# Optimization experiments

Hardware: AMD Instinct MI355X
Metric: run time of the kernel (lower is better)

## Reference

```python
import jax, jax.numpy as jnp
import numpy as np
from jax import lax

H_SIZE = 2048
NUM_K = 16
NUM_V = 32
DK = 128
DV = 128
KDIM = NUM_K * DK      # 2048
VDIM = NUM_V * DV      # 4096
KCONV = 4
RMS_EPS = 1e-6
L2_EPS = 1e-6


def l2norm(x, eps=L2_EPS):
    # matches torch l2norm: x * rsqrt(sum(x^2, -1) + eps)
    return x * lax.rsqrt(jnp.sum(x * x, axis=-1, keepdims=True) + eps)


def setup_inputs() -> dict:
    key = jax.random.key(0)
    ks = jax.random.split(key, 7)
    B, S = 2, 1024
    conv_dim = 2 * KDIM + VDIM  # 8192
    return {
        "hidden_states": jax.random.normal(ks[0], (B, S, H_SIZE), jnp.float32),
        "w_qkvz": jax.random.normal(ks[1], (H_SIZE, 2 * KDIM + 2 * VDIM), jnp.float32) * 0.02,
        "w_ba": jax.random.normal(ks[2], (H_SIZE, 2 * NUM_V), jnp.float32) * 0.02,
        "conv_w": jax.random.normal(ks[3], (conv_dim, 1, KCONV), jnp.float32) * 0.2,  # depthwise [C,1,K]
        "dt_bias": jnp.ones((NUM_V,), jnp.float32),
        "A_log": jnp.log(jax.random.uniform(ks[4], (NUM_V,), jnp.float32, 0.5, 8.0)),
        "norm_w": jnp.ones((DV,), jnp.float32),
        "w_out": jax.random.normal(ks[5], (VDIM, H_SIZE), jnp.float32) * 0.02,
    }


def _forward(hidden_states, w_qkvz, w_ba, conv_w, dt_bias, A_log, norm_w, w_out):
    B, S, _ = hidden_states.shape
    rf = NUM_V // NUM_K  # GQA repeat factor = 2

    # input projections
    qkvz = hidden_states @ w_qkvz                                  # [B,S,12288]
    ba = hidden_states @ w_ba                                      # [B,S,64]

    # fix_query_key_value_ordering: group per k-head then split
    qkvz = qkvz.reshape(B, S, NUM_K, 2 * DK + 2 * rf * DV)
    q, k, v, z = jnp.split(qkvz, [DK, 2 * DK, 2 * DK + rf * DV], axis=3)
    ba = ba.reshape(B, S, NUM_K, 2 * rf)
    b, a = jnp.split(ba, [rf], axis=3)
    v = v.reshape(B, S, NUM_V, DV)
    z = z.reshape(B, S, NUM_V, DV)
    b = b.reshape(B, S, NUM_V)
    a = a.reshape(B, S, NUM_V)

    # depthwise causal conv over [q|k|v] channels + silu
    mixed = jnp.concatenate(
        [q.reshape(B, S, KDIM), k.reshape(B, S, KDIM), v.reshape(B, S, VDIM)], axis=-1
    )                                                              # [B,S,conv_dim]
    x = mixed.transpose(0, 2, 1)                                   # [B,C,S]
    x = jnp.pad(x, ((0, 0), (0, 0), (KCONV - 1, 0)))
    x = lax.conv_general_dilated(x, conv_w, window_strides=(1,), padding="VALID",
                                 feature_group_count=x.shape[1])
    x = jax.nn.silu(x).transpose(0, 2, 1)                          # [B,S,conv_dim]

    q, k, v = jnp.split(x, [KDIM, 2 * KDIM], axis=-1)
    q = q.reshape(B, S, NUM_K, DK)
    k = k.reshape(B, S, NUM_K, DK)
    v = v.reshape(B, S, NUM_V, DV)

    beta = jax.nn.sigmoid(b)                                       # [B,S,NUM_V]
    g = -jnp.exp(A_log) * jax.nn.softplus(a + dt_bias)             # log-decay [B,S,NUM_V]

    if rf > 1:
        q = jnp.repeat(q, rf, axis=2)                              # [B,S,NUM_V,DK]
        k = jnp.repeat(k, rf, axis=2)
    q = l2norm(q) * (DK ** -0.5)
    k = l2norm(k)

    # gated delta rule recurrence over time via lax.scan
    S0 = jnp.zeros((B, NUM_V, DK, DV), q.dtype)

    def step(state, inp):
        q_t, k_t, v_t, g_t, b_t = inp                              # [B,H,dk]/[B,H,dv]/[B,H]
        state = state * jnp.exp(g_t)[..., None, None]              # decay
        kv_mem = jnp.einsum("bhkv,bhk->bhv", state, k_t)
        delta = (v_t - kv_mem) * b_t[..., None]
        state = state + jnp.einsum("bhk,bhv->bhkv", k_t, delta)
        o = jnp.einsum("bhkv,bhk->bhv", state, q_t)
        return state, o

    xs = (jnp.moveaxis(q, 1, 0), jnp.moveaxis(k, 1, 0), jnp.moveaxis(v, 1, 0),
          jnp.moveaxis(g, 1, 0), jnp.moveaxis(beta, 1, 0))
    _, out = lax.scan(step, S0, xs)
    out = jnp.moveaxis(out, 0, 1)                                  # [B,S,NUM_V,DV]

    # gated RMSNorm (gate applied before normalization, Mamba2 style)
    xg = out * jax.nn.silu(z)
    y = xg * lax.rsqrt(jnp.mean(xg * xg, axis=-1, keepdims=True) + RMS_EPS) * norm_w
    y = y.reshape(B, S, VDIM)
    return y @ w_out                                               # [B,S,H_SIZE]


def reference(hidden_states, w_qkvz, w_ba, conv_w, dt_bias, A_log, norm_w, w_out):
    return _forward(hidden_states, w_qkvz, w_ba, conv_w, dt_bias, A_log, norm_w, w_out)
```

## Files before the change

### kernel.cpp

```cpp
#include <hip/hip_runtime.h>
#include <stdint.h>

#define AS1 __attribute__((address_space(1)))
#define AS3 __attribute__((address_space(3)))

typedef __bf16 bf16x8 __attribute__((ext_vector_type(8)));
typedef float f32x4 __attribute__((ext_vector_type(4)));

static __device__ __forceinline__ float bf2f(unsigned short u) {
    union { unsigned int i; float f; } x; x.i = ((unsigned int)u) << 16; return x.f;
}
static __device__ __forceinline__ unsigned short f2bf(float f) {
    union { float f; unsigned int i; } x; x.f = f;
    unsigned int u = x.i;
    unsigned int r = (u + 0x7fffu + ((u >> 16) & 1u)) >> 16;
    return (unsigned short)r;
}

static __device__ __forceinline__ void gll16(const void* g, void* l) {
    __builtin_amdgcn_global_load_lds((const AS1 unsigned int*)g,
                                     (AS3 unsigned int*)l, 16, 0, 0);
}

__global__ __launch_bounds__(256) void cvt_bf16_kernel(
    const float* __restrict__ src, unsigned short* __restrict__ dst, int n4) {
    int i = blockIdx.x * 256 + threadIdx.x;
    if (i >= n4) return;
    float4 v = ((const float4*)src)[i];
    ushort4 o;
    o.x = f2bf(v.x); o.y = f2bf(v.y); o.z = f2bf(v.z); o.w = f2bf(v.w);
    ((ushort4*)dst)[i] = o;
}

__global__ __launch_bounds__(256) void transpose_cvt_kernel(
    const float* __restrict__ src, unsigned short* __restrict__ dst, int R, int C) {
    __shared__ float tile[32][33];
    int x = threadIdx.x & 31, y = threadIdx.x >> 5;
    int c0 = blockIdx.x * 32, r0 = blockIdx.y * 32;
#pragma unroll
    for (int i = 0; i < 4; i++)
        tile[y + i * 8][x] = src[(size_t)(r0 + y + i * 8) * C + (c0 + x)];
    __syncthreads();
#pragma unroll
    for (int i = 0; i < 4; i++)
        dst[(size_t)(c0 + y + i * 8) * R + (r0 + x)] = f2bf(tile[x][y + i * 8]);
}

template <int STORE_BF16>
__global__ __launch_bounds__(256) void gemm_bt_kernel(
    const unsigned short* __restrict__ A, const unsigned short* __restrict__ Bt,
    void* __restrict__ C, int M, int N, int K) {
    __shared__ __align__(16) unsigned short As[128 * 32];
    __shared__ __align__(16) unsigned short Bs[128 * 32];
    int tid = threadIdx.x;
    int lane = tid & 63;
    int w = tid >> 6;
    int m0 = blockIdx.y * 128;
    int n0 = blockIdx.x * 128;
    int qd = lane >> 4, rc = lane & 15;
    int wm = (w >> 1) * 64, wn = (w & 1) * 64;

    f32x4 acc[4][4];
#pragma unroll
    for (int i = 0; i < 4; i++)
#pragma unroll
        for (int j = 0; j < 4; j++)
#pragma unroll
            for (int r = 0; r < 4; r++) acc[i][j][r] = 0.f;

    int s0 = w * 128 + lane;
    int s1 = s0 + 64;
    int rA0 = s0 >> 2, cs0 = (s0 & 3) * 8;
    int rA1 = s1 >> 2, cs1 = (s1 & 3) * 8;
    const unsigned short* a0 = A + (size_t)(m0 + rA0) * K + cs0;
    const unsigned short* a1 = A + (size_t)(m0 + rA1) * K + cs1;
    const unsigned short* b0 = Bt + (size_t)(n0 + rA0) * K + cs0;
    const unsigned short* b1 = Bt + (size_t)(n0 + rA1) * K + cs1;
    unsigned short* lA0 = As + s0 * 8;
    unsigned short* lA1 = As + s1 * 8;
    unsigned short* lB0 = Bs + s0 * 8;
    unsigned short* lB1 = Bs + s1 * 8;

    for (int k0 = 0; k0 < K; k0 += 32) {
        __syncthreads();
        gll16(a0 + k0, lA0);
        gll16(a1 + k0, lA1);
        gll16(b0 + k0, lB0);
        gll16(b1 + k0, lB1);
        __syncthreads();
        bf16x8 af[4], bfr[4];
#pragma unroll
        for (int i = 0; i < 4; i++)
            af[i] = *(const bf16x8*)(As + (wm + i * 16 + rc) * 32 + qd * 8);
#pragma unroll
        for (int i = 0; i < 4; i++)
            bfr[i] = *(const bf16x8*)(Bs + (wn + i * 16 + rc) * 32 + qd * 8);
#pragma unroll
        for (int i = 0; i < 4; i++)
#pragma unroll
            for (int j = 0; j < 4; j++)
                acc[i][j] = __builtin_amdgcn_mfma_f32_16x16x32_bf16(af[i], bfr[j], acc[i][j], 0, 0, 0);
    }

#pragma unroll
    for (int i = 0; i < 4; i++)
#pragma unroll
        for (int j = 0; j < 4; j++)
#pragma unroll
            for (int r = 0; r < 4; r++) {
                int row = m0 + wm + i * 16 + qd * 4 + r;
                int col = n0 + wn + j * 16 + rc;
                if (STORE_BF16)
                    ((unsigned short*)C)[(size_t)row * N + col] = f2bf(acc[i][j][r]);
                else
                    ((float*)C)[(size_t)row * N + col] = acc[i][j][r];
            }
}

__global__ __launch_bounds__(256) void bag_kernel(
    const float* __restrict__ hs, const float* __restrict__ w_ba,
    const float* __restrict__ A_log, const float* __restrict__ dt_bias,
    float* __restrict__ gg, float* __restrict__ bb) {
    int w = threadIdx.x >> 6, lane = threadIdx.x & 63;
    int r0 = blockIdx.x * 8 + w * 2;
    const float* h0 = hs + (size_t)r0 * 2048;
    float a0 = 0.f, a1 = 0.f;
    for (int k = 0; k < 2048; k++) {
        float wv = w_ba[k * 64 + lane];
        a0 += h0[k] * wv;
        a1 += h0[2048 + k] * wv;
    }
    int h = lane >> 2, idx = lane & 3;
    int vh = h * 2 + (idx & 1);
    float accs[2] = {a0, a1};
#pragma unroll
    for (int j = 0; j < 2; j++) {
        int t = r0 + j;
        float acc = accs[j];
        if (idx < 2) {
            bb[t * 32 + vh] = 1.f / (1.f + expf(-acc));
        } else {
            float x = acc + dt_bias[vh];
            float sp = fmaxf(x, 0.f) + log1pf(expf(-fabsf(x)));
            gg[t * 32 + vh] = -expf(A_log[vh]) * sp;
        }
    }
}

__global__ __launch_bounds__(256) void conv_kernel(
    const unsigned short* __restrict__ qkvz, const float* __restrict__ conv_w,
    unsigned short* __restrict__ qb, unsigned short* __restrict__ kb,
    float* __restrict__ vv) {
    __shared__ float xs[8192];
    __shared__ float rs[32];
    int t = blockIdx.x;
    int s = t & 1023;
    int tid = threadIdx.x;
    size_t rowbase = (size_t)t * 12288;
#pragma unroll
    for (int i = 0; i < 4; i++) {
        int c = (i * 256 + tid) * 8;
        int d = c & 127;
        int col;
        if (c < 2048) col = (c >> 7) * 768 + d;
        else if (c < 4096) col = ((c - 2048) >> 7) * 768 + 128 + d;
        else { int vh2 = (c - 4096) >> 7; col = (vh2 >> 1) * 768 + 256 + (vh2 & 1) * 128 + d; }
        float wts[8][4];
#pragma unroll
        for (int e = 0; e < 8; e++) {
            float4 t4 = *(const float4*)(conv_w + (size_t)(c + e) * 4);
            wts[e][0] = t4.x; wts[e][1] = t4.y; wts[e][2] = t4.z; wts[e][3] = t4.w;
        }
        float acc[8] = {0.f, 0.f, 0.f, 0.f, 0.f, 0.f, 0.f, 0.f};
#pragma unroll
        for (int j = 0; j < 4; j++) {
            int ss = s - 3 + j;
            if (ss >= 0) {
                uint4 u = *(const uint4*)(qkvz + rowbase + (size_t)(j - 3) * 12288 + col);
                const unsigned short* us = (const unsigned short*)&u;
#pragma unroll
                for (int e = 0; e < 8; e++) acc[e] += bf2f(us[e]) * wts[e][j];
            }
        }
#pragma unroll
        for (int e = 0; e < 8; e++) xs[c + e] = acc[e] / (1.f + expf(-acc[e]));
    }
    __syncthreads();
    {
        int seg = tid >> 3, part = tid & 7;
        const float* pp = xs + seg * 128 + part * 16;
        float s2 = 0.f;
#pragma unroll
        for (int j = 0; j < 16; j++) s2 += pp[j] * pp[j];
        s2 += __shfl_xor(s2, 1);
        s2 += __shfl_xor(s2, 2);
        s2 += __shfl_xor(s2, 4);
        if (part == 0) rs[seg] = rsqrtf(s2 + 1e-6f);
    }
    __syncthreads();
    const float QS = 0.08838834764831845f;
#pragma unroll
    for (int i = 0; i < 4; i++) {
        int c = (i * 256 + tid) * 8;
        float x[8];
#pragma unroll
        for (int e = 0; e < 8; e++) x[e] = xs[c + e];
        if (c < 4096) {
            float sc = (c < 2048) ? rs[c >> 7] * QS : rs[((c - 2048) >> 7) + 16];
            uint4 o;
            o.x = (unsigned)f2bf(x[0] * sc) | ((unsigned)f2bf(x[1] * sc) << 16);
            o.y = (unsigned)f2bf(x[2] * sc) | ((unsigned)f2bf(x[3] * sc) << 16);
            o.z = (unsigned)f2bf(x[4] * sc) | ((unsigned)f2bf(x[5] * sc) << 16);
            o.w = (unsigned)f2bf(x[6] * sc) | ((unsigned)f2bf(x[7] * sc) << 16);
            if (c < 2048) *(uint4*)(qb + (size_t)t * 2048 + c) = o;
            else *(uint4*)(kb + (size_t)t * 2048 + c - 2048) = o;
        } else {
            float* vp = vv + (size_t)t * 4096 + c - 4096;
            *(float4*)vp = make_float4(x[0], x[1], x[2], x[3]);
            *(float4*)(vp + 4) = make_float4(x[4], x[5], x[6], x[7]);
        }
    }
}

__global__ __launch_bounds__(256, 2) void prep_kernel(
    const unsigned short* __restrict__ qb, const unsigned short* __restrict__ kb,
    const float* __restrict__ vv, const float* __restrict__ gg,
    const float* __restrict__ bb,
    unsigned short* __restrict__ Wg, unsigned short* __restrict__ DlT,
    unsigned short* __restrict__ KtT, unsigned short* __restrict__ Pt,
    float* __restrict__ lamg, float* __restrict__ l64g) {
    __shared__ __align__(16) unsigned short Ks[64 * 136];
    __shared__ __align__(16) unsigned short Tb[64 * 72];
    __shared__ __align__(16) unsigned short Xb[64 * 72];
    __shared__ float Td[4 * 16 * 17];
    __shared__ float RHS[64 * 68];
    __shared__ float cc[64], bet[64], lam_s[64], ex64[64];

    int bid = blockIdx.x;
    int ch = bid & 15, bh = bid >> 4;
    int vh = bh & 31, b = bh >> 5;
    int hk = vh >> 1;
    int t0 = b * 1024 + ch * 64;
    int tid = threadIdx.x, wv = tid >> 6, lane = tid & 63;
    int qd = lane >> 4, rc = lane & 15;
    int rowb = (wv & 1) * 32;
    size_t obase = (size_t)bid * 8192;
    size_t pbase = (size_t)bid * 4096;

    {
        int tok = tid >> 2, seg = (tid & 3) * 32;
        const unsigned short* src = kb + ((size_t)(t0 + tok) * 16 + hk) * 128 + seg;
#pragma unroll
        for (int j = 0; j < 4; j++) {
            uint4 u = *(const uint4*)(src + j * 8);
            *(uint4*)&Ks[tok * 136 + seg + j * 8] = u;
        }
    }
    if (tid < 64) {
        float x = gg[(size_t)(t0 + tid) * 32 + vh];
#pragma unroll
        for (int ofs = 1; ofs < 64; ofs <<= 1) {
            float up = __shfl_up(x, ofs, 64);
            if (tid >= ofs) x += up;
        }
        cc[tid] = x;
        float l = __expf(x);
        lam_s[tid] = l;
        float tot = __shfl(x, 63, 64);
        ex64[tid] = __expf(tot - x);
        bet[tid] = bb[(size_t)(t0 + tid) * 32 + vh];
        lamg[(size_t)bid * 64 + tid] = l;
        if (tid == 0) l64g[bid] = __expf(tot);
    }
    __syncthreads();

    {
        f32x4 acc[2][4];
#pragma unroll
        for (int tm = 0; tm < 2; tm++)
#pragma unroll
            for (int tn = 0; tn < 4; tn++)
#pragma unroll
                for (int r = 0; r < 4; r++) acc[tm][tn][r] = 0.f;
#pragma unroll
        for (int ks = 0; ks < 4; ks++) {
            bf16x8 af[2], bfr[4];
#pragma unroll
            for (int tm = 0; tm < 2; tm++) {
                int row = rowb + tm * 16 + rc;
                if (wv < 2)
                    af[tm] = *(const bf16x8*)&Ks[row * 136 + ks * 32 + qd * 8];
                else
                    af[tm] = *(const bf16x8*)(qb + ((size_t)(t0 + row) * 16 + hk) * 128 + ks * 32 + qd * 8);
            }
#pragma unroll
            for (int tn = 0; tn < 4; tn++)
                bfr[tn] = *(const bf16x8*)&Ks[(tn * 16 + rc) * 136 + ks * 32 + qd * 8];
#pragma unroll
            for (int tm = 0; tm < 2; tm++)
#pragma unroll
                for (int tn = 0; tn < 4; tn++)
                    acc[tm][tn] = __builtin_amdgcn_mfma_f32_16x16x32_bf16(af[tm], bfr[tn], acc[tm][tn], 0, 0, 0);
        }
        if (wv < 2) {
#pragma unroll
            for (int tm = 0; tm < 2; tm++)
#pragma unroll
                for (int tn = 0; tn < 4; tn++)
#pragma unroll
                    for (int r = 0; r < 4; r++) {
                        int i = rowb + tm * 16 + qd * 4 + r;
                        int j = tn * 16 + rc;
                        float val = acc[tm][tn][r];
                        float tv = 0.f;
                        if (i > j) tv = bet[i] * __expf(cc[i] - cc[j]) * val;
                        Tb[i * 72 + j] = f2bf(-tv);
                        if ((i >> 4) == (j >> 4) && i > j)
                            Td[(i >> 4) * 272 + (i & 15) * 17 + (j & 15)] = tv;
                    }
        } else {
#pragma unroll
            for (int tm = 0; tm < 2; tm++)
#pragma unroll
                for (int tn = 0; tn < 4; tn++)
#pragma unroll
                    for (int r = 0; r < 4; r++) {
                        int i = rowb + tm * 16 + qd * 4 + r;
                        int j = tn * 16 + rc;
                        float ev = (i >= j) ? __expf(cc[i] - cc[j]) : 0.f;
                        Pt[pbase + i * 64 + j] = f2bf(ev * acc[tm][tn][r]);
                    }
        }
    }
    {
        int dk = tid >> 1, half = tid & 1;
#pragma unroll
        for (int j = 0; j < 4; j++) {
            unsigned short tmp[8];
#pragma unroll
            for (int e = 0; e < 8; e++) {
                int tok = half * 32 + j * 8 + e;
                tmp[e] = f2bf(bf2f(Ks[tok * 136 + dk]) * ex64[tok]);
            }
            *(uint4*)(KtT + obase + dk * 64 + half * 32 + j * 8) = *(const uint4*)tmp;
        }
    }
    __syncthreads();

#pragma unroll 1
    for (int cb = 0; cb < 4; cb++) {
        for (int z = tid; z < 64 * 72 / 2; z += 256) ((unsigned int*)Xb)[z] = 0u;
        {
            int tok = tid >> 2, c0 = (tid & 3) * 16;
            if (cb < 2) {
                const float* vp = vv + ((size_t)(t0 + tok) * 32 + vh) * 128 + cb * 64 + c0;
                float bt = bet[tok];
#pragma unroll
                for (int j = 0; j < 4; j++) {
                    float4 v4 = *(const float4*)(vp + j * 4);
                    *(float4*)&RHS[tok * 68 + c0 + j * 4] =
                        make_float4(v4.x * bt, v4.y * bt, v4.z * bt, v4.w * bt);
                }
            } else {
                float bl = bet[tok] * lam_s[tok];
#pragma unroll
                for (int e = 0; e < 16; e++)
                    RHS[tok * 68 + c0 + e] = bl * bf2f(Ks[tok * 136 + (cb - 2) * 64 + c0 + e]);
            }
        }
        __syncthreads();
#pragma unroll
        for (int B = 0; B < 4; B++) {
            if (wv == B) {
                f32x4 tacc[4];
#pragma unroll
                for (int cf = 0; cf < 4; cf++)
#pragma unroll
                    for (int r = 0; r < 4; r++)
                        tacc[cf][r] = RHS[(B * 16 + qd * 4 + r) * 68 + cf * 16 + rc];
                const int nks = (B + 1) >> 1;
#pragma unroll
                for (int ks = 0; ks < 2; ks++) {
                    if (ks >= nks) break;
                    bf16x8 af = *(const bf16x8*)&Tb[(B * 16 + rc) * 72 + ks * 32 + qd * 8];
#pragma unroll
                    for (int cf = 0; cf < 4; cf++) {
                        bf16x8 bf_ = *(const bf16x8*)&Xb[(cf * 16 + rc) * 72 + ks * 32 + qd * 8];
                        tacc[cf] = __builtin_amdgcn_mfma_f32_16x16x32_bf16(af, bf_, tacc[cf], 0, 0, 0);
                    }
                }
#pragma unroll
                for (int cf = 0; cf < 4; cf++)
#pragma unroll
                    for (int r = 0; r < 4; r++)
                        RHS[(B * 16 + qd * 4 + r) * 68 + cf * 16 + rc] = tacc[cf][r];
                __builtin_amdgcn_s_waitcnt(0xc07f);
                {
                    float d[16];
#pragma unroll
                    for (int i2 = 0; i2 < 16; i2++) d[i2] = RHS[(B * 16 + i2) * 68 + lane];
#pragma unroll
                    for (int i2 = 1; i2 < 16; i2++)
#pragma unroll
                        for (int j2 = 0; j2 < i2; j2++)
                            d[i2] -= Td[B * 272 + i2 * 17 + j2] * d[j2];
#pragma unroll
                    for (int i2 = 0; i2 < 16; i2++)
                        Xb[lane * 72 + B * 16 + i2] = f2bf(d[i2]);
                }
            }
            __syncthreads();
        }
        if (cb < 2) {
            int cl = tid >> 2, tq = (tid & 3) * 16;
#pragma unroll
            for (int j = 0; j < 2; j++) {
                uint4 u = *(const uint4*)&Xb[cl * 72 + tq + j * 8];
                *(uint4*)(DlT + obase + (cb * 64 + cl) * 64 + tq + j * 8) = u;
            }
        } else {
            int tok = tid & 63, dq = tid >> 6;
#pragma unroll
            for (int j = 0; j < 2; j++) {
                unsigned short tmp[8];
#pragma unroll
                for (int e = 0; e < 8; e++)
                    tmp[e] = Xb[(dq * 16 + j * 8 + e) * 72 + tok];
                *(uint4*)(Wg + obase + tok * 128 + (cb - 2) * 64 + dq * 16 + j * 8) = *(const uint4*)tmp;
            }
        }
        __syncthreads();
    }
}

__global__ __launch_bounds__(256, 2) void recb_kernel(
    const unsigned short* __restrict__ qb, const float* __restrict__ lamg,
    const float* __restrict__ l64g, const unsigned short* __restrict__ Wg,
    const unsigned short* __restrict__ DlT, const unsigned short* __restrict__ KtT,
    const unsigned short* __restrict__ Pt, float* __restrict__ oo) {
    __shared__ __align__(16) unsigned short St[16 * 136];
    __shared__ __align__(16) unsigned short Dls[16 * 72];
    int bid = blockIdx.x;
    int slice = bid >> 6;
    int rest = bid & 63;
    int vh = rest & 31, b = rest >> 5;
    int bh = b * 32 + vh;
    int hk = vh >> 1, dvo = slice * 16, tb = b * 1024;
    int tid = threadIdx.x, wv = tid >> 6, lane = tid & 63;
    int qd = lane >> 4, rc = lane & 15;

    f32x4 sacc[2];
#pragma unroll
    for (int tm = 0; tm < 2; tm++)
#pragma unroll
        for (int r = 0; r < 4; r++) sacc[tm][r] = 0.f;
    for (int z = tid; z < 16 * 136 / 2; z += 256) ((unsigned int*)St)[z] = 0u;
    __syncthreads();

#pragma unroll 1
    for (int ch = 0; ch < 16; ch++) {
        int bhch = bh * 16 + ch;
        size_t obase = (size_t)bhch * 8192;
        size_t pbase = (size_t)bhch * 4096;
        int t0 = tb + ch * 64;
        if (tid < 128) {
            int row = tid >> 3, t8 = (tid & 7) * 8;
            uint4 u = *(const uint4*)(DlT + obase + (dvo + row) * 64 + t8);
            *(uint4*)&Dls[row * 72 + t8] = u;
        }
        __syncthreads();
        {
            f32x4 uacc;
#pragma unroll
            for (int r = 0; r < 4; r++) uacc[r] = 0.f;
#pragma unroll
            for (int ks = 0; ks < 4; ks++) {
                bf16x8 a_ = *(const bf16x8*)&St[rc * 136 + ks * 32 + qd * 8];
                bf16x8 b_ = *(const bf16x8*)(Wg + obase + (size_t)(wv * 16 + rc) * 128 + ks * 32 + qd * 8);
                uacc = __builtin_amdgcn_mfma_f32_16x16x32_bf16(a_, b_, uacc, 0, 0, 0);
            }
#pragma unroll
            for (int r = 0; r < 4; r++) {
                int idx = (qd * 4 + r) * 72 + wv * 16 + rc;
                Dls[idx] = f2bf(bf2f(Dls[idx]) - uacc[r]);
            }
        }
        __syncthreads();
        {
            f32x4 qacc;
#pragma unroll
            for (int r = 0; r < 4; r++) qacc[r] = 0.f;
#pragma unroll
            for (int ks = 0; ks < 4; ks++) {
                bf16x8 a_ = *(const bf16x8*)(qb + ((size_t)(t0 + wv * 16 + rc) * 16 + hk) * 128 + ks * 32 + qd * 8);
                bf16x8 b_ = *(const bf16x8*)&St[rc * 136 + ks * 32 + qd * 8];
                qacc = __builtin_amdgcn_mfma_f32_16x16x32_bf16(a_, b_, qacc, 0, 0, 0);
            }
            bf16x8 bd[2];
#pragma unroll
            for (int ks = 0; ks < 2; ks++)
                bd[ks] = *(const bf16x8*)&Dls[rc * 72 + ks * 32 + qd * 8];
            f32x4 oacc;
#pragma unroll
            for (int r = 0; r < 4; r++)
                oacc[r] = lamg[(size_t)bhch * 64 + wv * 16 + qd * 4 + r] * qacc[r];
#pragma unroll
            for (int ks = 0; ks < 2; ks++) {
                bf16x8 a_ = *(const bf16x8*)(Pt + pbase + (size_t)(wv * 16 + rc) * 64 + ks * 32 + qd * 8);
                oacc = __builtin_amdgcn_mfma_f32_16x16x32_bf16(a_, bd[ks], oacc, 0, 0, 0);
            }
#pragma unroll
            for (int r = 0; r < 4; r++)
                oo[((size_t)(t0 + wv * 16 + qd * 4 + r) * 32 + vh) * 128 + dvo + rc] = oacc[r];
            float l64 = l64g[bhch];
#pragma unroll
            for (int tm = 0; tm < 2; tm++) {
#pragma unroll
                for (int r = 0; r < 4; r++) sacc[tm][r] *= l64;
#pragma unroll
                for (int ks = 0; ks < 2; ks++) {
                    bf16x8 a_ = *(const bf16x8*)(KtT + obase + (size_t)(wv * 32 + tm * 16 + rc) * 64 + ks * 32 + qd * 8);
                    sacc[tm] = __builtin_amdgcn_mfma_f32_16x16x32_bf16(a_, bd[ks], sacc[tm], 0, 0, 0);
                }
            }
        }
        __syncthreads();
#pragma unroll
        for (int tm = 0; tm < 2; tm++)
#pragma unroll
            for (int r = 0; r < 4; r++)
                St[rc * 136 + wv * 32 + tm * 16 + qd * 4 + r] = f2bf(sacc[tm][r]);
        __syncthreads();
    }
}

__global__ __launch_bounds__(256) void norm_kernel(
    const float* __restrict__ oo, const unsigned short* __restrict__ qkvz,
    const float* __restrict__ norm_w, unsigned short* __restrict__ yb) {
    int w = threadIdx.x >> 6, lane = threadIdx.x & 63;
    int g = blockIdx.x * 4 + w;
    int t = g >> 5, vh = g & 31;
    size_t ob = (size_t)g * 128;
    size_t zb = (size_t)t * 12288 + (size_t)(vh >> 1) * 768 + 512 + (vh & 1) * 128;
    float x0 = oo[ob + lane], x1 = oo[ob + 64 + lane];
    float z0 = bf2f(qkvz[zb + lane]), z1 = bf2f(qkvz[zb + 64 + lane]);
    float xg0 = x0 * (z0 / (1.f + expf(-z0)));
    float xg1 = x1 * (z1 / (1.f + expf(-z1)));
    float s = xg0 * xg0 + xg1 * xg1;
    s += __shfl_xor(s, 1);
    s += __shfl_xor(s, 2);
    s += __shfl_xor(s, 4);
    s += __shfl_xor(s, 8);
    s += __shfl_xor(s, 16);
    s += __shfl_xor(s, 32);
    float r = rsqrtf(s * (1.f / 128.f) + 1e-6f);
    size_t y0 = (size_t)t * 4096 + (size_t)vh * 128;
    yb[y0 + lane] = f2bf(xg0 * r * norm_w[lane]);
    yb[y0 + 64 + lane] = f2bf(xg1 * r * norm_w[64 + lane]);
}

extern "C" void kernel_launch(void* const* d_in, const int* in_sizes, int n_in,
                              void* d_out, int out_size, void* d_ws, size_t ws_size,
                              hipStream_t stream) {
    const float* hs      = (const float*)d_in[0];
    const float* w_qkvz  = (const float*)d_in[1];
    const float* w_ba    = (const float*)d_in[2];
    const float* conv_w  = (const float*)d_in[3];
    const float* dt_bias = (const float*)d_in[4];
    const float* A_log   = (const float*)d_in[5];
    const float* norm_w  = (const float*)d_in[6];
    const float* w_out   = (const float*)d_in[7];
    float* out = (float*)d_out;
    (void)in_sizes; (void)n_in; (void)out_size; (void)ws_size;

    char* p = (char*)d_ws;
    auto alloc = [&](size_t b) { char* r = p; p += (b + 255) & ~(size_t)255; return r; };
    float* gg = (float*)alloc(2048ull * 32 * 4);
    float* bb = (float*)alloc(2048ull * 32 * 4);
    unsigned short* hsb  = (unsigned short*)alloc(2048ull * 2048 * 2);
    unsigned short* wqT  = (unsigned short*)alloc(12288ull * 2048 * 2);
    unsigned short* woT  = (unsigned short*)alloc(2048ull * 4096 * 2);
    unsigned short* qkvz = (unsigned short*)alloc(2048ull * 12288 * 2);
    unsigned short* qb16 = (unsigned short*)alloc(2048ull * 2048 * 2);
    unsigned short* kb16 = (unsigned short*)alloc(2048ull * 2048 * 2);
    float* vv = (float*)alloc(2048ull * 4096 * 4);
    float* oo = (float*)alloc(2048ull * 4096 * 4);
    unsigned short* yb = (unsigned short*)alloc(2048ull * 4096 * 2);
    unsigned short* Wg  = (unsigned short*)alloc(1024ull * 8192 * 2);
    unsigned short* DlT = (unsigned short*)alloc(1024ull * 8192 * 2);
    unsigned short* KtT = (unsigned short*)alloc(1024ull * 8192 * 2);
    unsigned short* Pt  = (unsigned short*)alloc(1024ull * 4096 * 2);
    float* lamg = (float*)alloc(1024ull * 64 * 4);
    float* l64g = (float*)alloc(1024ull * 4);

    cvt_bf16_kernel<<<4096, 256, 0, stream>>>(hs, hsb, 2048 * 2048 / 4);
    transpose_cvt_kernel<<<dim3(12288 / 32, 2048 / 32), 256, 0, stream>>>(w_qkvz, wqT, 2048, 12288);
    transpose_cvt_kernel<<<dim3(2048 / 32, 4096 / 32), 256, 0, stream>>>(w_out, woT, 4096, 2048);
    gemm_bt_kernel<1><<<dim3(96, 16), 256, 0, stream>>>(hsb, wqT, qkvz, 2048, 12288, 2048);
    bag_kernel<<<256, 256, 0, stream>>>(hs, w_ba, A_log, dt_bias, gg, bb);
    conv_kernel<<<2048, 256, 0, stream>>>(qkvz, conv_w, qb16, kb16, vv);
    prep_kernel<<<1024, 256, 0, stream>>>(qb16, kb16, vv, gg, bb, Wg, DlT, KtT, Pt, lamg, l64g);
    recb_kernel<<<512, 256, 0, stream>>>(qb16, lamg, l64g, Wg, DlT, KtT, Pt, oo);
    norm_kernel<<<16384, 256, 0, stream>>>(oo, qkvz, norm_w, yb);
    gemm_bt_kernel<0><<<dim3(16, 16), 256, 0, stream>>>(yb, woT, out, 2048, 2048, 4096);
}
```

Measured before the change: 784.6 us.

## Split-K output GEMM and parallelize prep triangular solves across waves

The output projection GEMM now runs with a split-K of two, writing fp32 partials into the reused wqT buffer, followed by a new reduction kernel that sums them into the output. This aims to fill more CUs, since the previous grid had only 256 blocks. In prep_kernel, each of the four waves now owns one column block of the blocked triangular solve, using private LDS scratch and reading K directly from global memory. This replaces the old serialized loop of 4x4 steps separated by block barriers, in exchange for more LDS and repeated global reads.

Result: faster. 761.5 us (-2.9%).

```diff
diff --git a/kernel.cpp b/kernel.cpp
--- a/kernel.cpp
+++ b/kernel.cpp
@@ -57,6 +57,8 @@
     int w = tid >> 6;
     int m0 = blockIdx.y * 128;
     int n0 = blockIdx.x * 128;
+    int zz = blockIdx.z;
+    int Kz = K / gridDim.z;
     int qd = lane >> 4, rc = lane & 15;
     int wm = (w >> 1) * 64, wn = (w & 1) * 64;
 
@@ -72,16 +74,16 @@
     int s1 = s0 + 64;
     int rA0 = s0 >> 2, cs0 = (s0 & 3) * 8;
     int rA1 = s1 >> 2, cs1 = (s1 & 3) * 8;
-    const unsigned short* a0 = A + (size_t)(m0 + rA0) * K + cs0;
-    const unsigned short* a1 = A + (size_t)(m0 + rA1) * K + cs1;
-    const unsigned short* b0 = Bt + (size_t)(n0 + rA0) * K + cs0;
-    const unsigned short* b1 = Bt + (size_t)(n0 + rA1) * K + cs1;
+    const unsigned short* a0 = A + (size_t)(m0 + rA0) * K + cs0 + (size_t)zz * Kz;
+    const unsigned short* a1 = A + (size_t)(m0 + rA1) * K + cs1 + (size_t)zz * Kz;
+    const unsigned short* b0 = Bt + (size_t)(n0 + rA0) * K + cs0 + (size_t)zz * Kz;
+    const unsigned short* b1 = Bt + (size_t)(n0 + rA1) * K + cs1 + (size_t)zz * Kz;
     unsigned short* lA0 = As + s0 * 8;
     unsigned short* lA1 = As + s1 * 8;
     unsigned short* lB0 = Bs + s0 * 8;
     unsigned short* lB1 = Bs + s1 * 8;
 
-    for (int k0 = 0; k0 < K; k0 += 32) {
+    for (int k0 = 0; k0 < Kz; k0 += 32) {
         __syncthreads();
         gll16(a0 + k0, lA0);
         gll16(a1 + k0, lA1);
@@ -113,8 +115,17 @@
                 if (STORE_BF16)
                     ((unsigned short*)C)[(size_t)row * N + col] = f2bf(acc[i][j][r]);
                 else
-                    ((float*)C)[(size_t)row * N + col] = acc[i][j][r];
-            }
+                    ((float*)C)[(size_t)zz * M * N + (size_t)row * N + col] = acc[i][j][r];
+            }
+}
+
+__global__ __launch_bounds__(256) void add_out_kernel(
+    const float* __restrict__ p, float* __restrict__ out, int n4) {
+    int i = blockIdx.x * 256 + threadIdx.x;
+    if (i >= n4) return;
+    float4 a = ((const float4*)p)[i];
+    float4 b = ((const float4*)(p + (size_t)n4 * 4))[i];
+    ((float4*)out)[i] = make_float4(a.x + b.x, a.y + b.y, a.z + b.z, a.w + b.w);
 }
 
 __global__ __launch_bounds__(256) void bag_kernel(
@@ -229,11 +240,10 @@
     unsigned short* __restrict__ Wg, unsigned short* __restrict__ DlT,
     unsigned short* __restrict__ KtT, unsigned short* __restrict__ Pt,
     float* __restrict__ lamg, float* __restrict__ l64g) {
-    __shared__ __align__(16) unsigned short Ks[64 * 136];
     __shared__ __align__(16) unsigned short Tb[64 * 72];
-    __shared__ __align__(16) unsigned short Xb[64 * 72];
+    __shared__ __align__(16) unsigned short Xw[4][64 * 72];
     __shared__ float Td[4 * 16 * 17];
-    __shared__ float RHS[64 * 68];
+    __shared__ float RHSw[4][16 * 68];
     __shared__ float cc[64], bet[64], lam_s[64], ex64[64];
 
     int bid = blockIdx.x;
@@ -247,15 +257,6 @@
     size_t obase = (size_t)bid * 8192;
     size_t pbase = (size_t)bid * 4096;
 
-    {
-        int tok = tid >> 2, seg = (tid & 3) * 32;
-        const unsigned short* src = kb + ((size_t)(t0 + tok) * 16 + hk) * 128 + seg;
-#pragma unroll
-        for (int j = 0; j < 4; j++) {
-            uint4 u = *(const uint4*)(src + j * 8);
-            *(uint4*)&Ks[tok * 136 + seg + j * 8] = u;
-        }
-    }
     if (tid < 64) {
         float x = gg[(size_t)(t0 + tid) * 32 + vh];
 #pragma unroll
@@ -275,6 +276,7 @@
     __syncthreads();
 
     {
+        const unsigned short* src = (wv >= 2) ? qb : kb;
         f32x4 acc[2][4];
 #pragma unroll
         for (int tm = 0; tm < 2; tm++)
@@ -288,14 +290,11 @@
 #pragma unroll
             for (int tm = 0; tm < 2; tm++) {
                 int row = rowb + tm * 16 + rc;
-                if (wv < 2)
-                    af[tm] = *(const bf16x8*)&Ks[row * 136 + ks * 32 + qd * 8];
-                else
-                    af[tm] = *(const bf16x8*)(qb + ((size_t)(t0 + row) * 16 + hk) * 128 + ks * 32 + qd * 8);
+                af[tm] = *(const bf16x8*)(src + ((size_t)(t0 + row) * 16 + hk) * 128 + ks * 32 + qd * 8);
             }
 #pragma unroll
             for (int tn = 0; tn < 4; tn++)
-                bfr[tn] = *(const bf16x8*)&Ks[(tn * 16 + rc) * 136 + ks * 32 + qd * 8];
+                bfr[tn] = *(const bf16x8*)(kb + ((size_t)(t0 + tn * 16 + rc) * 16 + hk) * 128 + ks * 32 + qd * 8);
 #pragma unroll
             for (int tm = 0; tm < 2; tm++)
 #pragma unroll
@@ -340,96 +339,83 @@
 #pragma unroll
             for (int e = 0; e < 8; e++) {
                 int tok = half * 32 + j * 8 + e;
-                tmp[e] = f2bf(bf2f(Ks[tok * 136 + dk]) * ex64[tok]);
+                tmp[e] = f2bf(bf2f(kb[((size_t)(t0 + tok) * 16 + hk) * 128 + dk]) * ex64[tok]);
             }
             *(uint4*)(KtT + obase + dk * 64 + half * 32 + j * 8) = *(const uint4*)tmp;
         }
     }
     __syncthreads();
 
-#pragma unroll 1
-    for (int cb = 0; cb < 4; cb++) {
-        for (int z = tid; z < 64 * 72 / 2; z += 256) ((unsigned int*)Xb)[z] = 0u;
-        {
-            int tok = tid >> 2, c0 = (tid & 3) * 16;
-            if (cb < 2) {
-                const float* vp = vv + ((size_t)(t0 + tok) * 32 + vh) * 128 + cb * 64 + c0;
-                float bt = bet[tok];
-#pragma unroll
-                for (int j = 0; j < 4; j++) {
-                    float4 v4 = *(const float4*)(vp + j * 4);
-                    *(float4*)&RHS[tok * 68 + c0 + j * 4] =
-                        make_float4(v4.x * bt, v4.y * bt, v4.z * bt, v4.w * bt);
+    {
+        int cb = wv;
+        unsigned short* Xb = Xw[wv];
+        float* RHS = RHSw[wv];
+        for (int z = lane; z < 64 * 72 / 2; z += 64) ((unsigned int*)Xb)[z] = 0u;
+#pragma unroll
+        for (int B = 0; B < 4; B++) {
+            f32x4 tacc[4];
+#pragma unroll
+            for (int cf = 0; cf < 4; cf++)
+#pragma unroll
+                for (int r = 0; r < 4; r++) {
+                    int i = B * 16 + qd * 4 + r;
+                    int c = cf * 16 + rc;
+                    float v;
+                    if (cb < 2)
+                        v = bet[i] * vv[((size_t)(t0 + i) * 32 + vh) * 128 + cb * 64 + c];
+                    else
+                        v = bet[i] * lam_s[i] * bf2f(kb[((size_t)(t0 + i) * 16 + hk) * 128 + (cb - 2) * 64 + c]);
+                    tacc[cf][r] = v;
                 }
-            } else {
-                float bl = bet[tok] * lam_s[tok];
-#pragma unroll
-                for (int e = 0; e < 16; e++)
-                    RHS[tok * 68 + c0 + e] = bl * bf2f(Ks[tok * 136 + (cb - 2) * 64 + c0 + e]);
-            }
-        }
-        __syncthreads();
-#pragma unroll
-        for (int B = 0; B < 4; B++) {
-            if (wv == B) {
-                f32x4 tacc[4];
-#pragma unroll
-                for (int cf = 0; cf < 4; cf++)
-#pragma unroll
-                    for (int r = 0; r < 4; r++)
-                        tacc[cf][r] = RHS[(B * 16 + qd * 4 + r) * 68 + cf * 16 + rc];
-                const int nks = (B + 1) >> 1;
-#pragma unroll
-                for (int ks = 0; ks < 2; ks++) {
-                    if (ks >= nks) break;
-                    bf16x8 af = *(const bf16x8*)&Tb[(B * 16 + rc) * 72 + ks * 32 + qd * 8];
-#pragma unroll
-                    for (int cf = 0; cf < 4; cf++) {
-                        bf16x8 bf_ = *(const bf16x8*)&Xb[(cf * 16 + rc) * 72 + ks * 32 + qd * 8];
-                        tacc[cf] = __builtin_amdgcn_mfma_f32_16x16x32_bf16(af, bf_, tacc[cf], 0, 0, 0);
-                    }
+            __builtin_amdgcn_s_waitcnt(0xc07f);
+            const int nks = (B + 1) >> 1;
+#pragma unroll
+            for (int ks = 0; ks < 2; ks++) {
+                if (ks >= nks) break;
+                bf16x8 af = *(const bf16x8*)&Tb[(B * 16 + rc) * 72 + ks * 32 + qd * 8];
+#pragma unroll
+                for (int cf = 0; cf < 4; cf++) {
+                    bf16x8 bf_ = *(const bf16x8*)&Xb[(cf * 16 + rc) * 72 + ks * 32 + qd * 8];
+                    tacc[cf] = __builtin_amdgcn_mfma_f32_16x16x32_bf16(af, bf_, tacc[cf], 0, 0, 0);
                 }
-#pragma unroll
-                for (int cf = 0; cf < 4; cf++)
-#pragma unroll
-                    for (int r = 0; r < 4; r++)
-                        RHS[(B * 16 + qd * 4 + r) * 68 + cf * 16 + rc] = tacc[cf][r];
-                __builtin_amdgcn_s_waitcnt(0xc07f);
-                {
-                    float d[16];
-#pragma unroll
-                    for (int i2 = 0; i2 < 16; i2++) d[i2] = RHS[(B * 16 + i2) * 68 + lane];
-#pragma unroll
-                    for (int i2 = 1; i2 < 16; i2++)
-#pragma unroll
-                        for (int j2 = 0; j2 < i2; j2++)
-                            d[i2] -= Td[B * 272 + i2 * 17 + j2] * d[j2];
-#pragma unroll
-                    for (int i2 = 0; i2 < 16; i2++)
-                        Xb[lane * 72 + B * 16 + i2] = f2bf(d[i2]);
-                }
-            }
-            __syncthreads();
-        }
+            }
+#pragma unroll
+            for (int cf = 0; cf < 4; cf++)
+#pragma unroll
+                for (int r = 0; r < 4; r++)
+                    RHS[(qd * 4 + r) * 68 + cf * 16 + rc] = tacc[cf][r];
+            __builtin_amdgcn_s_waitcnt(0xc07f);
+            {
+                float d[16];
+#pragma unroll
+                for (int i2 = 0; i2 < 16; i2++) d[i2] = RHS[i2 * 68 + lane];
+#pragma unroll
+                for (int i2 = 1; i2 < 16; i2++)
+#pragma unroll
+                    for (int j2 = 0; j2 < i2; j2++)
+                        d[i2] -= Td[B * 272 + i2 * 17 + j2] * d[j2];
+#pragma unroll
+                for (int i2 = 0; i2 < 16; i2++)
+                    Xb[lane * 72 + B * 16 + i2] = f2bf(d[i2]);
+            }
+        }
+        __builtin_amdgcn_s_waitcnt(0xc07f);
         if (cb < 2) {
-            int cl = tid >> 2, tq = (tid & 3) * 16;
-#pragma unroll
-            for (int j = 0; j < 2; j++) {
-                uint4 u = *(const uint4*)&Xb[cl * 72 + tq + j * 8];
-                *(uint4*)(DlT + obase + (cb * 64 + cl) * 64 + tq + j * 8) = u;
+#pragma unroll
+            for (int j = 0; j < 8; j++) {
+                uint4 u = *(const uint4*)&Xb[lane * 72 + j * 8];
+                *(uint4*)(DlT + obase + (size_t)(cb * 64 + lane) * 64 + j * 8) = u;
             }
         } else {
-            int tok = tid & 63, dq = tid >> 6;
-#pragma unroll
-            for (int j = 0; j < 2; j++) {
+#pragma unroll
+            for (int dq = 0; dq < 8; dq++) {
                 unsigned short tmp[8];
 #pragma unroll
                 for (int e = 0; e < 8; e++)
-                    tmp[e] = Xb[(dq * 16 + j * 8 + e) * 72 + tok];
-                *(uint4*)(Wg + obase + tok * 128 + (cb - 2) * 64 + dq * 16 + j * 8) = *(const uint4*)tmp;
-            }
-        }
-        __syncthreads();
+                    tmp[e] = Xb[(dq * 8 + e) * 72 + lane];
+                *(uint4*)(Wg + obase + (size_t)lane * 128 + (cb - 2) * 64 + dq * 8) = *(const uint4*)tmp;
+            }
+        }
     }
 }
 
@@ -592,15 +578,17 @@
     unsigned short* Pt  = (unsigned short*)alloc(1024ull * 4096 * 2);
     float* lamg = (float*)alloc(1024ull * 64 * 4);
     float* l64g = (float*)alloc(1024ull * 4);
+    float* gpart = (float*)wqT;
 
     cvt_bf16_kernel<<<4096, 256, 0, stream>>>(hs, hsb, 2048 * 2048 / 4);
     transpose_cvt_kernel<<<dim3(12288 / 32, 2048 / 32), 256, 0, stream>>>(w_qkvz, wqT, 2048, 12288);
     transpose_cvt_kernel<<<dim3(2048 / 32, 4096 / 32), 256, 0, stream>>>(w_out, woT, 4096, 2048);
-    gemm_bt_kernel<1><<<dim3(96, 16), 256, 0, stream>>>(hsb, wqT, qkvz, 2048, 12288, 2048);
+    gemm_bt_kernel<1><<<dim3(96, 16, 1), 256, 0, stream>>>(hsb, wqT, qkvz, 2048, 12288, 2048);
     bag_kernel<<<256, 256, 0, stream>>>(hs, w_ba, A_log, dt_bias, gg, bb);
     conv_kernel<<<2048, 256, 0, stream>>>(qkvz, conv_w, qb16, kb16, vv);
     prep_kernel<<<1024, 256, 0, stream>>>(qb16, kb16, vv, gg, bb, Wg, DlT, KtT, Pt, lamg, l64g);
     recb_kernel<<<512, 256, 0, stream>>>(qb16, lamg, l64g, Wg, DlT, KtT, Pt, oo);
     norm_kernel<<<16384, 256, 0, stream>>>(oo, qkvz, norm_w, yb);
-    gemm_bt_kernel<0><<<dim3(16, 16), 256, 0, stream>>>(yb, woT, out, 2048, 2048, 4096);
-}
+    gemm_bt_kernel<0><<<dim3(16, 16, 2), 256, 0, stream>>>(yb, woT, gpart, 2048, 2048, 4096);
+    add_out_kernel<<<4096, 256, 0, stream>>>(gpart, out, 2048 * 2048 / 4);
+}
```
